# Performance work log

Hardware: AMD Instinct MI355X
Metric: run time of the kernel (lower is better)

The kernel has to match this reference:

```python
import jax, jax.numpy as jnp
import numpy as np

N_NODES = 50000
N_EDGES = 800000
NODE_DIM = 10
EDGE_DIM = 5
HID = 64


def _tconv(x, src, dst, e_attr, wq, bq, wk, bk, wv, bv, we, ws, bs):
    # PyG TransformerConv, heads=1, concat=True, root_weight=True, beta=False
    n = x.shape[0]
    q = x @ wq + bq                      # [N, HID]
    k = x @ wk + bk                      # [N, HID]
    v = x @ wv + bv                      # [N, HID]
    ee = e_attr @ we                     # [E, HID] (lin_edge, no bias)
    ke = k[src] + ee                     # key per edge
    ve = v[src] + ee                     # value per edge
    logits = jnp.sum(q[dst] * ke, axis=-1) / 8.0  # sqrt(64) = 8
    m = jax.ops.segment_max(logits, dst, num_segments=n)
    p = jnp.exp(logits - m[dst])
    s = jax.ops.segment_sum(p, dst, num_segments=n)
    alpha = p / s[dst]                   # segment softmax over in-neighbors
    agg = jax.ops.segment_sum(alpha[:, None] * ve, dst, num_segments=n)
    return agg + x @ ws + bs             # + lin_skip(x_i)


def setup_inputs() -> dict:
    key = jax.random.key(0)
    ks = jax.random.split(key, 32)
    x = jax.random.uniform(ks[0], (N_NODES, NODE_DIM), dtype=jnp.float32)
    edge_index = jax.random.randint(ks[1], (2, N_EDGES), 0, N_NODES, dtype=jnp.int64)
    edge_attr = jax.random.uniform(ks[2], (N_EDGES, EDGE_DIM), dtype=jnp.float32)

    def lin(k, fan_in, fan_out):
        b = 1.0 / np.sqrt(fan_in)
        return jax.random.uniform(k, (fan_in, fan_out), jnp.float32, -b, b)

    def bias(k, fan_in, fan_out):
        b = 1.0 / np.sqrt(fan_in)
        return jax.random.uniform(k, (fan_out,), jnp.float32, -b, b)

    inp = dict(x=x, edge_index=edge_index, edge_attr=edge_attr)
    # conv1: NODE_DIM -> HID
    inp['w1q'] = lin(ks[3], NODE_DIM, HID); inp['b1q'] = bias(ks[4], NODE_DIM, HID)
    inp['w1k'] = lin(ks[5], NODE_DIM, HID); inp['b1k'] = bias(ks[6], NODE_DIM, HID)
    inp['w1v'] = lin(ks[7], NODE_DIM, HID); inp['b1v'] = bias(ks[8], NODE_DIM, HID)
    inp['w1e'] = lin(ks[9], EDGE_DIM, HID)
    inp['w1s'] = lin(ks[10], NODE_DIM, HID); inp['b1s'] = bias(ks[11], NODE_DIM, HID)
    # 5 stacked HID -> HID layers
    inp['wq'] = jnp.stack([lin(jax.random.fold_in(ks[12], i), HID, HID) for i in range(5)])
    inp['bq'] = jnp.stack([bias(jax.random.fold_in(ks[13], i), HID, HID) for i in range(5)])
    inp['wk'] = jnp.stack([lin(jax.random.fold_in(ks[14], i), HID, HID) for i in range(5)])
    inp['bk'] = jnp.stack([bias(jax.random.fold_in(ks[15], i), HID, HID) for i in range(5)])
    inp['wv'] = jnp.stack([lin(jax.random.fold_in(ks[16], i), HID, HID) for i in range(5)])
    inp['bv'] = jnp.stack([bias(jax.random.fold_in(ks[17], i), HID, HID) for i in range(5)])
    inp['we'] = jnp.stack([lin(jax.random.fold_in(ks[18], i), EDGE_DIM, HID) for i in range(5)])
    inp['ws'] = jnp.stack([lin(jax.random.fold_in(ks[19], i), HID, HID) for i in range(5)])
    inp['bs'] = jnp.stack([bias(jax.random.fold_in(ks[20], i), HID, HID) for i in range(5)])
    # final linear HID -> 1
    inp['lin_w'] = lin(ks[21], HID, 1); inp['lin_b'] = bias(ks[22], HID, 1)
    return inp


def reference(x, edge_index, edge_attr, w1q, b1q, w1k, b1k, w1v, b1v, w1e, w1s, b1s,
              wq, bq, wk, bk, wv, bv, we, ws, bs, lin_w, lin_b):
    src, dst = edge_index[0], edge_index[1]  # x_j = x[src], aggregated into dst
    h = jnp.log(x + 1.0)
    e = jnp.log(edge_attr + 1.0)
    h = _tconv(h, src, dst, e, w1q, b1q, w1k, b1k, w1v, b1v, w1e, w1s, b1s)
    for i in range(5):
        h = _tconv(h, src, dst, e, wq[i], bq[i], wk[i], bk[i], wv[i], bv[i], we[i], ws[i], bs[i])
    return h @ lin_w + lin_b  # [N, 1]
```

## Files before the change

### kernel.cpp

```cpp
#include <hip/hip_runtime.h>
#include <hip/hip_fp16.h>
#include <cstdint>
#include <cstddef>

#define NN 50000
#define NE 800000
#define HD 64
#define SB 49

__global__ void k_hist(const int* __restrict__ ei, int* __restrict__ cnt) {
    int e = blockIdx.x * blockDim.x + threadIdx.x;
    if (e < NE) atomicAdd(&cnt[ei[NE + e]], 1);
}

__global__ __launch_bounds__(256) void k_scan1(const int* __restrict__ cnt,
                                               int* __restrict__ row_start,
                                               int* __restrict__ bsum) {
    __shared__ int ssum[256];
    const int tid = threadIdx.x, b = blockIdx.x;
    const int i0 = b * 1024 + tid * 4;
    int c0 = 0, c1 = 0, c2 = 0, c3 = 0;
    if (i0 + 3 < NN) {
        const int4 c = *(const int4*)(cnt + i0);
        c0 = c.x; c1 = c.y; c2 = c.z; c3 = c.w;
    } else {
        if (i0 + 0 < NN) c0 = cnt[i0 + 0];
        if (i0 + 1 < NN) c1 = cnt[i0 + 1];
        if (i0 + 2 < NN) c2 = cnt[i0 + 2];
        if (i0 + 3 < NN) c3 = cnt[i0 + 3];
    }
    ssum[tid] = c0 + c1 + c2 + c3;
    __syncthreads();
    for (int off = 1; off < 256; off <<= 1) {
        int v = (tid >= off) ? ssum[tid - off] : 0;
        __syncthreads();
        ssum[tid] += v;
        __syncthreads();
    }
    int ex = (tid == 0) ? 0 : ssum[tid - 1];
    if (i0 + 0 < NN) row_start[i0 + 0] = ex;
    ex += c0;
    if (i0 + 1 < NN) row_start[i0 + 1] = ex;
    ex += c1;
    if (i0 + 2 < NN) row_start[i0 + 2] = ex;
    ex += c2;
    if (i0 + 3 < NN) row_start[i0 + 3] = ex;
    if (tid == 255) bsum[b] = ssum[255];
}

__global__ __launch_bounds__(64) void k_scan2(const int* __restrict__ bsum,
                                              int* __restrict__ boff,
                                              int* __restrict__ row_start) {
    __shared__ int s[64];
    const int t = threadIdx.x;
    s[t] = (t < SB) ? bsum[t] : 0;
    __syncthreads();
    for (int off = 1; off < 64; off <<= 1) {
        int v = (t >= off) ? s[t - off] : 0;
        __syncthreads();
        s[t] += v;
        __syncthreads();
    }
    if (t < SB) boff[t] = (t == 0) ? 0 : s[t - 1];
    if (t == 0) row_start[NN] = s[SB - 1];
}

__global__ __launch_bounds__(256) void k_scan3(int* __restrict__ row_start,
                                               const int* __restrict__ boff,
                                               int* __restrict__ cur) {
    const int b = blockIdx.x;
    const int i0 = b * 1024 + threadIdx.x * 4;
    const int o = boff[b];
#pragma unroll
    for (int k = 0; k < 4; ++k) {
        int i = i0 + k;
        if (i < NN) {
            int v = row_start[i] + o;
            row_start[i] = v;
            cur[i] = v;
        }
    }
}

__global__ void k_scatter(const int* __restrict__ ei, const float* __restrict__ ea,
                          int* __restrict__ cur, uint4* __restrict__ e5p) {
    int e = blockIdx.x * blockDim.x + threadIdx.x;
    if (e < NE) {
        int d = ei[NE + e];
        int pos = atomicAdd(&cur[d], 1);
        const float e0 = __logf(ea[(size_t)e * 5 + 0] + 1.f);
        const float e1 = __logf(ea[(size_t)e * 5 + 1] + 1.f);
        const float e2 = __logf(ea[(size_t)e * 5 + 2] + 1.f);
        const float e3 = __logf(ea[(size_t)e * 5 + 3] + 1.f);
        const float e4 = __logf(ea[(size_t)e * 5 + 4] + 1.f);
        union { __half2 h; unsigned u; } c01, c23;
        c01.h = __floats2half2_rn(e0, e1);
        c23.h = __floats2half2_rn(e2, e3);
        uint4 rec;
        rec.x = c01.u;
        rec.y = c23.u;
        rec.z = ((unsigned)ei[e] << 16) |
                (unsigned)__half_as_ushort(__float2half_rn(e4));
        rec.w = 0u;
        e5p[pos] = rec;
    }
}

__device__ __forceinline__ void cvt_kv(const uint4 u, float4& k4, float4& v4) {
    const float2 p0 = __half22float2(*(const __half2*)&u.x);
    const float2 p1 = __half22float2(*(const __half2*)&u.y);
    const float2 p2 = __half22float2(*(const __half2*)&u.z);
    const float2 p3 = __half22float2(*(const __half2*)&u.w);
    k4 = make_float4(p0.x, p1.x, p2.x, p3.x);
    v4 = make_float4(p0.y, p1.y, p2.y, p3.y);
}

__global__ __launch_bounds__(256, 4) void k_qkvs10(
    const float* __restrict__ x,
    const float* __restrict__ Wq, const float* __restrict__ Bq,
    const float* __restrict__ Wk, const float* __restrict__ Bk,
    const float* __restrict__ Wv, const float* __restrict__ Bv,
    const float* __restrict__ Ws, const float* __restrict__ Bs,
    float* __restrict__ qb, __half* __restrict__ kvh, float* __restrict__ sb) {
    __shared__ float xs[640];
    const int lane = threadIdx.x & 63;
    const int w = threadIdx.x >> 6;
    const bool iskv = (w == 1 || w == 3);
    const float* WA = (w == 0) ? Wq : iskv ? Wk : Ws;
    const float* BA = (w == 0) ? Bq : iskv ? Bk : Bs;
    const float scl = (w == 0) ? 0.125f : 1.f;
    float wrA[10], wrB[10];
#pragma unroll
    for (int j = 0; j < 10; ++j) {
        wrA[j] = WA[j * 64 + lane] * scl;
        wrB[j] = iskv ? Wv[j * 64 + lane] : 0.f;
    }
    const float bA = BA[lane] * scl;
    const float bB = iskv ? Bv[lane] : 0.f;
    const int tile = blockIdx.x;
    const int fbase = tile * 640;
    const int fcnt = min(640, NN * 10 - fbase);
    if (threadIdx.x * 4 < fcnt) {
        float4 v = *(const float4*)(x + (size_t)fbase + threadIdx.x * 4);
        v.x = __logf(v.x + 1.f);
        v.y = __logf(v.y + 1.f);
        v.z = __logf(v.z + 1.f);
        v.w = __logf(v.w + 1.f);
        *(float4*)&xs[threadIdx.x * 4] = v;
    }
    __syncthreads();
    const int nbase = tile * 64;
    const int nodes = min(64, NN - nbase);
    const int n0 = (w == 3) ? 32 : 0;
    const int n1 = iskv ? ((w == 1) ? min(nodes, 32) : nodes) : nodes;
    for (int n = n0; n < n1; ++n) {
        float accA = bA, accB = bB;
#pragma unroll
        for (int j = 0; j < 10; ++j) {
            const float xv = xs[n * 10 + j];
            accA = fmaf(xv, wrA[j], accA);
            accB = fmaf(xv, wrB[j], accB);
        }
        const size_t node = (size_t)(nbase + n);
        if (iskv) {
            const __half2 hv = __floats2half2_rn(accA, accB);
            *(__half2*)(kvh + node * 128 + lane * 2) = hv;
        } else if (w == 0) {
            qb[node * 64 + lane] = accA;
        } else {
            sb[node * 64 + lane] = accA;
        }
    }
}

template <bool FINAL>
__global__ __launch_bounds__(256) void k_agg(
    const float* __restrict__ q, const __half* __restrict__ kv,
    const float* __restrict__ sk, const uint4* __restrict__ e5p,
    const float* __restrict__ wE, const int* __restrict__ row_start,
    float* __restrict__ hout, const float* __restrict__ lw, const float* lb,
    const float* __restrict__ Wq, const float* __restrict__ Bq,
    const float* __restrict__ Wk, const float* __restrict__ Bk,
    const float* __restrict__ Wv, const float* __restrict__ Bv,
    const float* __restrict__ Ws, const float* __restrict__ Bs,
    float* __restrict__ qout, __half* __restrict__ kvout,
    float* __restrict__ sout) {
    __shared__ float ols[256];
    __shared__ float kls[256];
    const int lane = threadIdx.x & 63;
    const int wave = threadIdx.x >> 6;
    const int g = lane >> 4, t = lane & 15;
    const int node = __builtin_amdgcn_readfirstlane(blockIdx.x * 4 + wave);
    const int beg = row_start[node], end = row_start[node + 1];
    const float4 s4 = *(const float4*)(sk + (size_t)node * 64 + t * 4);
    float4 o4;
    if (beg == end) {
        o4 = s4;
    } else {
        const float4 q4 = *(const float4*)(q + (size_t)node * 64 + t * 4);
        float g5[5];
        {
            const float4 wg = *(const float4*)(wE + g * 64 + t * 4);
            float dc = q4.x * wg.x;
            dc = fmaf(q4.y, wg.y, dc);
            dc = fmaf(q4.z, wg.z, dc);
            dc = fmaf(q4.w, wg.w, dc);
            dc += __shfl_xor(dc, 1);
            dc += __shfl_xor(dc, 2);
            dc += __shfl_xor(dc, 4);
            dc += __shfl_xor(dc, 8);
            const float4 w4 = *(const float4*)(wE + 4 * 64 + t * 4);
            float d4 = q4.x * w4.x;
            d4 = fmaf(q4.y, w4.y, d4);
            d4 = fmaf(q4.z, w4.z, d4);
            d4 = fmaf(q4.w, w4.w, d4);
            d4 += __shfl_xor(d4, 1);
            d4 += __shfl_xor(d4, 2);
            d4 += __shfl_xor(d4, 4);
            d4 += __shfl_xor(d4, 8);
            g5[0] = __shfl(dc, 0);
            g5[1] = __shfl(dc, 16);
            g5[2] = __shfl(dc, 32);
            g5[3] = __shfl(dc, 48);
            g5[4] = __shfl(d4, 0);
        }
        float m = -1e30f, l = 0.f;
        float4 accv = {0.f, 0.f, 0.f, 0.f};
        float a50 = 0.f, a51 = 0.f, a52 = 0.f, a53 = 0.f, a54 = 0.f;
        const char* kvc = (const char*)kv;
        const int i0x = beg + g;
        const int i0 = (i0x < end) ? i0x : beg;
        uint4 r0 = e5p[i0];
        const int i1x = beg + 4 + g;
        const int i1 = (i1x < end) ? i1x : beg;
        uint4 r1 = e5p[i1];
        uint4 kv8 =
            *(const uint4*)(kvc + (size_t)((r0.z & 0xffff0000u) >> 8) + t * 16);
#pragma unroll 2
        for (int p = beg; p < end; p += 4) {
            const int nx = p + 8 + g;
            const int npp = (nx < end) ? nx : beg;
            const uint4 rn = e5p[npp];
            const uint4 nkv =
                *(const uint4*)(kvc + (size_t)((r1.z & 0xffff0000u) >> 8) + t * 16);
            const bool act = (p + g) < end;
            float4 k4, v4;
            cvt_kv(kv8, k4, v4);
            const float2 e01 = __half22float2(*(const __half2*)&r0.x);
            const float2 e23 = __half22float2(*(const __half2*)&r0.y);
            const float e4v =
                __half2float(__ushort_as_half((unsigned short)(r0.z & 0xffffu)));
            float d = q4.x * k4.x;
            d = fmaf(q4.y, k4.y, d);
            d = fmaf(q4.z, k4.z, d);
            d = fmaf(q4.w, k4.w, d);
            d += __shfl_xor(d, 1);
            d += __shfl_xor(d, 2);
            d += __shfl_xor(d, 4);
            d += __shfl_xor(d, 8);
            float d5 = g5[0] * e01.x;
            d5 = fmaf(g5[1], e01.y, d5);
            d5 = fmaf(g5[2], e23.x, d5);
            d5 = fmaf(g5[3], e23.y, d5);
            d5 = fmaf(g5[4], e4v, d5);
            const float la = act ? (d + d5) : -__builtin_inff();
            float pa = __expf(la - m);
            if (la > m + 8.f) {
                const float rs = __expf(m - la);
                l *= rs;
                accv.x *= rs;
                accv.y *= rs;
                accv.z *= rs;
                accv.w *= rs;
                a50 *= rs;
                a51 *= rs;
                a52 *= rs;
                a53 *= rs;
                a54 *= rs;
                m = la;
                pa = 1.f;
            }
            l += pa;
            accv.x = fmaf(pa, v4.x, accv.x);
            accv.y = fmaf(pa, v4.y, accv.y);
            accv.z = fmaf(pa, v4.z, accv.z);
            accv.w = fmaf(pa, v4.w, accv.w);
            a50 = fmaf(pa, e01.x, a50);
            a51 = fmaf(pa, e01.y, a51);
            a52 = fmaf(pa, e23.x, a52);
            a53 = fmaf(pa, e23.y, a53);
            a54 = fmaf(pa, e4v, a54);
            r0 = r1;
            r1 = rn;
            kv8 = nkv;
        }
        float M = fmaxf(m, __shfl_xor(m, 16));
        M = fmaxf(M, __shfl_xor(M, 32));
        const float f = __expf(m - M);
        float lz = l * f;
        lz += __shfl_xor(lz, 16);
        lz += __shfl_xor(lz, 32);
        accv.x *= f;
        accv.y *= f;
        accv.z *= f;
        accv.w *= f;
        a50 *= f;
        a51 *= f;
        a52 *= f;
        a53 *= f;
        a54 *= f;
#pragma unroll
        for (int s = 16; s <= 32; s <<= 1) {
            accv.x += __shfl_xor(accv.x, s);
            accv.y += __shfl_xor(accv.y, s);
            accv.z += __shfl_xor(accv.z, s);
            accv.w += __shfl_xor(accv.w, s);
            a50 += __shfl_xor(a50, s);
            a51 += __shfl_xor(a51, s);
            a52 += __shfl_xor(a52, s);
            a53 += __shfl_xor(a53, s);
            a54 += __shfl_xor(a54, s);
        }
        float4 t4 = accv;
        {
            const float4 w0 = *(const float4*)(wE + 0 * 64 + t * 4);
            const float4 w1 = *(const float4*)(wE + 1 * 64 + t * 4);
            const float4 w2 = *(const float4*)(wE + 2 * 64 + t * 4);
            const float4 w3 = *(const float4*)(wE + 3 * 64 + t * 4);
            const float4 w4r = *(const float4*)(wE + 4 * 64 + t * 4);
            t4.x = fmaf(a50, w0.x, t4.x);
            t4.y = fmaf(a50, w0.y, t4.y);
            t4.z = fmaf(a50, w0.z, t4.z);
            t4.w = fmaf(a50, w0.w, t4.w);
            t4.x = fmaf(a51, w1.x, t4.x);
            t4.y = fmaf(a51, w1.y, t4.y);
            t4.z = fmaf(a51, w1.z, t4.z);
            t4.w = fmaf(a51, w1.w, t4.w);
            t4.x = fmaf(a52, w2.x, t4.x);
            t4.y = fmaf(a52, w2.y, t4.y);
            t4.z = fmaf(a52, w2.z, t4.z);
            t4.w = fmaf(a52, w2.w, t4.w);
            t4.x = fmaf(a53, w3.x, t4.x);
            t4.y = fmaf(a53, w3.y, t4.y);
            t4.z = fmaf(a53, w3.z, t4.z);
            t4.w = fmaf(a53, w3.w, t4.w);
            t4.x = fmaf(a54, w4r.x, t4.x);
            t4.y = fmaf(a54, w4r.y, t4.y);
            t4.z = fmaf(a54, w4r.z, t4.z);
            t4.w = fmaf(a54, w4r.w, t4.w);
        }
        const float rl = 1.f / lz;
        o4.x = fmaf(t4.x, rl, s4.x);
        o4.y = fmaf(t4.y, rl, s4.y);
        o4.z = fmaf(t4.z, rl, s4.z);
        o4.w = fmaf(t4.w, rl, s4.w);
    }
    if (FINAL) {
        const float4 lw4 = *(const float4*)(lw + t * 4);
        float r = o4.x * lw4.x;
        r = fmaf(o4.y, lw4.y, r);
        r = fmaf(o4.z, lw4.z, r);
        r = fmaf(o4.w, lw4.w, r);
        r += __shfl_xor(r, 1);
        r += __shfl_xor(r, 2);
        r += __shfl_xor(r, 4);
        r += __shfl_xor(r, 8);
        if (lane == 0) hout[node] = r + lb[0];
        return;
    }
    if (g == 0) *(float4*)&ols[wave * 64 + t * 4] = o4;
    __syncthreads();
    const float* W = (wave == 0) ? Wq : (wave == 1) ? Ws : (wave == 2) ? Wk : Wv;
    const float* B = (wave == 0) ? Bq : (wave == 1) ? Bs : (wave == 2) ? Bk : Bv;
    const float scl = (wave == 0) ? 0.125f : 1.f;
    float wr[64];
#pragma unroll
    for (int j = 0; j < 64; ++j) wr[j] = W[j * 64 + lane] * scl;
    const float bias = B[lane] * scl;
    float acc[4] = {bias, bias, bias, bias};
#pragma unroll
    for (int jq = 0; jq < 16; ++jq) {
#pragma unroll
        for (int n = 0; n < 4; ++n) {
            const float4 xv = *(const float4*)&ols[n * 64 + jq * 4];
            acc[n] = fmaf(xv.x, wr[jq * 4 + 0], acc[n]);
            acc[n] = fmaf(xv.y, wr[jq * 4 + 1], acc[n]);
            acc[n] = fmaf(xv.z, wr[jq * 4 + 2], acc[n]);
            acc[n] = fmaf(xv.w, wr[jq * 4 + 3], acc[n]);
        }
    }
    if (wave == 2) {
#pragma unroll
        for (int n = 0; n < 4; ++n) kls[n * 64 + lane] = acc[n];
    }
    __syncthreads();
    const int nb = blockIdx.x * 4;
    if (wave == 0) {
#pragma unroll
        for (int n = 0; n < 4; ++n) qout[(size_t)(nb + n) * 64 + lane] = acc[n];
    } else if (wave == 1) {
#pragma unroll
        for (int n = 0; n < 4; ++n) sout[(size_t)(nb + n) * 64 + lane] = acc[n];
    } else if (wave == 3) {
#pragma unroll
        for (int n = 0; n < 4; ++n) {
            const float kk = kls[n * 64 + lane];
            *(__half2*)(kvout + (size_t)(nb + n) * 128 + lane * 2) =
                __floats2half2_rn(kk, acc[n]);
        }
    }
}

extern "C" void kernel_launch(void* const* d_in, const int* in_sizes, int n_in,
                              void* d_out, int out_size, void* d_ws, size_t ws_size,
                              hipStream_t stream) {
    const float* x = (const float*)d_in[0];
    const int* ei = (const int*)d_in[1];
    const float* ea = (const float*)d_in[2];
    const float* w1q = (const float*)d_in[3];
    const float* b1q = (const float*)d_in[4];
    const float* w1k = (const float*)d_in[5];
    const float* b1k = (const float*)d_in[6];
    const float* w1v = (const float*)d_in[7];
    const float* b1v = (const float*)d_in[8];
    const float* w1e = (const float*)d_in[9];
    const float* w1s = (const float*)d_in[10];
    const float* b1s = (const float*)d_in[11];
    const float* wq = (const float*)d_in[12];
    const float* bq = (const float*)d_in[13];
    const float* wk = (const float*)d_in[14];
    const float* bk = (const float*)d_in[15];
    const float* wv = (const float*)d_in[16];
    const float* bv = (const float*)d_in[17];
    const float* we = (const float*)d_in[18];
    const float* ws = (const float*)d_in[19];
    const float* bs = (const float*)d_in[20];
    const float* lw = (const float*)d_in[21];
    const float* lb = (const float*)d_in[22];

    uintptr_t p = (uintptr_t)d_ws;
    auto alloc = [&](size_t bytes) -> void* {
        void* r = (void*)p;
        p += (bytes + 255) & ~(size_t)255;
        return r;
    };
    uint4* e5p = (uint4*)alloc((size_t)NE * 16);
    float* qA = (float*)alloc((size_t)NN * HD * 4);
    float* qB = (float*)alloc((size_t)NN * HD * 4);
    float* sA = (float*)alloc((size_t)NN * HD * 4);
    float* sB = (float*)alloc((size_t)NN * HD * 4);
    __half* kvA = (__half*)alloc((size_t)NN * 128 * 2);
    __half* kvB = (__half*)alloc((size_t)NN * 128 * 2);
    int* row_start = (int*)alloc((size_t)(NN + 1) * 4);
    int* cnt = (int*)alloc((size_t)NN * 4);
    int* cur = (int*)alloc((size_t)NN * 4);
    int* bsum = (int*)alloc((size_t)SB * 4);
    int* boff = (int*)alloc((size_t)SB * 4);

    hipMemsetAsync(cnt, 0, (size_t)NN * 4, stream);
    k_hist<<<(NE + 255) / 256, 256, 0, stream>>>(ei, cnt);
    k_scan1<<<SB, 256, 0, stream>>>(cnt, row_start, bsum);
    k_scan2<<<1, 64, 0, stream>>>(bsum, boff, row_start);
    k_scan3<<<SB, 256, 0, stream>>>(row_start, boff, cur);
    k_scatter<<<(NE + 255) / 256, 256, 0, stream>>>(ei, ea, cur, e5p);

    const int gg10 = (NN + 63) / 64;
    const int agg_grid = NN / 4;

    k_qkvs10<<<gg10, 256, 0, stream>>>(x, w1q, b1q, w1k, b1k, w1v, b1v, w1s, b1s,
                                       qA, kvA, sA);

    const float* wEs[6] = {w1e, we, we + 320, we + 640, we + 960, we + 1280};
    float* qin = qA;  float* qo = qB;
    float* sin_ = sA; float* so = sB;
    __half* kvin = kvA; __half* kvo = kvB;
    for (int k = 0; k < 5; ++k) {
        k_agg<false><<<agg_grid, 256, 0, stream>>>(
            qin, kvin, sin_, e5p, wEs[k], row_start, nullptr, lw, lb,
            wq + k * 4096, bq + k * 64, wk + k * 4096, bk + k * 64,
            wv + k * 4096, bv + k * 64, ws + k * 4096, bs + k * 64,
            qo, kvo, so);
        float* tf;  __half* th;
        tf = qin; qin = qo; qo = tf;
        tf = sin_; sin_ = so; so = tf;
        th = kvin; kvin = kvo; kvo = th;
    }
    k_agg<true><<<agg_grid, 256, 0, stream>>>(
        qin, kvin, sin_, e5p, wEs[5], row_start, (float*)d_out, lw, lb,
        wq, bq, wk, bk, wv, bv, ws, bs, qo, kvo, so);
}
```

Measured before the change: 620.9 us.

## Make aggregation kernel persistent and hoist per-wave weight loads out of node loop

The per-layer aggregation kernel becomes a grid-stride persistent kernel with 1024 blocks, each looping over groups of four nodes. The 64 per-lane weight registers for the fused next-layer projection are loaded once per block instead of once per four nodes, which cuts repeated weight traffic. Launch bounds now ask for 4 blocks per CU, which can constrain registers and cause spills given the 64-float weight array kept live across the loop. A fixed grid may also balance uneven node degrees worse than a large one-shot grid.

```diff
diff --git a/kernel.cpp b/kernel.cpp
--- a/kernel.cpp
+++ b/kernel.cpp
@@ -7,6 +7,7 @@
 #define NE 800000
 #define HD 64
 #define SB 49
+#define NQUAD 12500
 
 __global__ void k_hist(const int* __restrict__ ei, int* __restrict__ cnt) {
     int e = blockIdx.x * blockDim.x + threadIdx.x;
@@ -174,7 +175,7 @@
 }
 
 template <bool FINAL>
-__global__ __launch_bounds__(256) void k_agg(
+__global__ __launch_bounds__(256, 4) void k_agg(
     const float* __restrict__ q, const __half* __restrict__ kv,
     const float* __restrict__ sk, const uint4* __restrict__ e5p,
     const float* __restrict__ wE, const int* __restrict__ row_start,
@@ -190,223 +191,228 @@
     const int lane = threadIdx.x & 63;
     const int wave = threadIdx.x >> 6;
     const int g = lane >> 4, t = lane & 15;
-    const int node = __builtin_amdgcn_readfirstlane(blockIdx.x * 4 + wave);
-    const int beg = row_start[node], end = row_start[node + 1];
-    const float4 s4 = *(const float4*)(sk + (size_t)node * 64 + t * 4);
-    float4 o4;
-    if (beg == end) {
-        o4 = s4;
-    } else {
-        const float4 q4 = *(const float4*)(q + (size_t)node * 64 + t * 4);
-        float g5[5];
-        {
-            const float4 wg = *(const float4*)(wE + g * 64 + t * 4);
-            float dc = q4.x * wg.x;
-            dc = fmaf(q4.y, wg.y, dc);
-            dc = fmaf(q4.z, wg.z, dc);
-            dc = fmaf(q4.w, wg.w, dc);
-            dc += __shfl_xor(dc, 1);
-            dc += __shfl_xor(dc, 2);
-            dc += __shfl_xor(dc, 4);
-            dc += __shfl_xor(dc, 8);
-            const float4 w4 = *(const float4*)(wE + 4 * 64 + t * 4);
-            float d4 = q4.x * w4.x;
-            d4 = fmaf(q4.y, w4.y, d4);
-            d4 = fmaf(q4.z, w4.z, d4);
-            d4 = fmaf(q4.w, w4.w, d4);
-            d4 += __shfl_xor(d4, 1);
-            d4 += __shfl_xor(d4, 2);
-            d4 += __shfl_xor(d4, 4);
-            d4 += __shfl_xor(d4, 8);
-            g5[0] = __shfl(dc, 0);
-            g5[1] = __shfl(dc, 16);
-            g5[2] = __shfl(dc, 32);
-            g5[3] = __shfl(dc, 48);
-            g5[4] = __shfl(d4, 0);
-        }
-        float m = -1e30f, l = 0.f;
-        float4 accv = {0.f, 0.f, 0.f, 0.f};
-        float a50 = 0.f, a51 = 0.f, a52 = 0.f, a53 = 0.f, a54 = 0.f;
-        const char* kvc = (const char*)kv;
-        const int i0x = beg + g;
-        const int i0 = (i0x < end) ? i0x : beg;
-        uint4 r0 = e5p[i0];
-        const int i1x = beg + 4 + g;
-        const int i1 = (i1x < end) ? i1x : beg;
-        uint4 r1 = e5p[i1];
-        uint4 kv8 =
-            *(const uint4*)(kvc + (size_t)((r0.z & 0xffff0000u) >> 8) + t * 16);
+    float wr[64];
+    float bias = 0.f;
+    if (!FINAL) {
+        const float* W = (wave == 0) ? Wq : (wave == 1) ? Ws : (wave == 2) ? Wk : Wv;
+        const float* B = (wave == 0) ? Bq : (wave == 1) ? Bs : (wave == 2) ? Bk : Bv;
+        const float wscl = (wave == 0) ? 0.125f : 1.f;
+#pragma unroll
+        for (int j = 0; j < 64; ++j) wr[j] = W[j * 64 + lane] * wscl;
+        bias = B[lane] * wscl;
+    }
+    for (int quad = blockIdx.x; quad < NQUAD; quad += gridDim.x) {
+        const int node = __builtin_amdgcn_readfirstlane(quad * 4 + wave);
+        const int beg = row_start[node], end = row_start[node + 1];
+        const float4 s4 = *(const float4*)(sk + (size_t)node * 64 + t * 4);
+        float4 o4;
+        if (beg == end) {
+            o4 = s4;
+        } else {
+            const float4 q4 = *(const float4*)(q + (size_t)node * 64 + t * 4);
+            float g5[5];
+            {
+                const float4 wg = *(const float4*)(wE + g * 64 + t * 4);
+                float dc = q4.x * wg.x;
+                dc = fmaf(q4.y, wg.y, dc);
+                dc = fmaf(q4.z, wg.z, dc);
+                dc = fmaf(q4.w, wg.w, dc);
+                dc += __shfl_xor(dc, 1);
+                dc += __shfl_xor(dc, 2);
+                dc += __shfl_xor(dc, 4);
+                dc += __shfl_xor(dc, 8);
+                const float4 w4 = *(const float4*)(wE + 4 * 64 + t * 4);
+                float d4 = q4.x * w4.x;
+                d4 = fmaf(q4.y, w4.y, d4);
+                d4 = fmaf(q4.z, w4.z, d4);
+                d4 = fmaf(q4.w, w4.w, d4);
+                d4 += __shfl_xor(d4, 1);
+                d4 += __shfl_xor(d4, 2);
+                d4 += __shfl_xor(d4, 4);
+                d4 += __shfl_xor(d4, 8);
+                g5[0] = __shfl(dc, 0);
+                g5[1] = __shfl(dc, 16);
+                g5[2] = __shfl(dc, 32);
+                g5[3] = __shfl(dc, 48);
+                g5[4] = __shfl(d4, 0);
+            }
+            float m = -1e30f, l = 0.f;
+            float4 accv = {0.f, 0.f, 0.f, 0.f};
+            float a50 = 0.f, a51 = 0.f, a52 = 0.f, a53 = 0.f, a54 = 0.f;
+            const char* kvc = (const char*)kv;
+            const int i0x = beg + g;
+            const int i0 = (i0x < end) ? i0x : beg;
+            uint4 r0 = e5p[i0];
+            const int i1x = beg + 4 + g;
+            const int i1 = (i1x < end) ? i1x : beg;
+            uint4 r1 = e5p[i1];
+            uint4 kv8 =
+                *(const uint4*)(kvc + (size_t)((r0.z & 0xffff0000u) >> 8) + t * 16);
 #pragma unroll 2
-        for (int p = beg; p < end; p += 4) {
-            const int nx = p + 8 + g;
-            const int npp = (nx < end) ? nx : beg;
-            const uint4 rn = e5p[npp];
-            const uint4 nkv =
-                *(const uint4*)(kvc + (size_t)((r1.z & 0xffff0000u) >> 8) + t * 16);
-            const bool act = (p + g) < end;
-            float4 k4, v4;
-            cvt_kv(kv8, k4, v4);
-            const float2 e01 = __half22float2(*(const __half2*)&r0.x);
-            const float2 e23 = __half22float2(*(const __half2*)&r0.y);
-            const float e4v =
-                __half2float(__ushort_as_half((unsigned short)(r0.z & 0xffffu)));
-            float d = q4.x * k4.x;
-            d = fmaf(q4.y, k4.y, d);
-            d = fmaf(q4.z, k4.z, d);
-            d = fmaf(q4.w, k4.w, d);
-            d += __shfl_xor(d, 1);
-            d += __shfl_xor(d, 2);
-            d += __shfl_xor(d, 4);
-            d += __shfl_xor(d, 8);
-            float d5 = g5[0] * e01.x;
-            d5 = fmaf(g5[1], e01.y, d5);
-            d5 = fmaf(g5[2], e23.x, d5);
-            d5 = fmaf(g5[3], e23.y, d5);
-            d5 = fmaf(g5[4], e4v, d5);
-            const float la = act ? (d + d5) : -__builtin_inff();
-            float pa = __expf(la - m);
-            if (la > m + 8.f) {
-                const float rs = __expf(m - la);
-                l *= rs;
-                accv.x *= rs;
-                accv.y *= rs;
-                accv.z *= rs;
-                accv.w *= rs;
-                a50 *= rs;
-                a51 *= rs;
-                a52 *= rs;
-                a53 *= rs;
-                a54 *= rs;
-                m = la;
-                pa = 1.f;
-            }
-            l += pa;
-            accv.x = fmaf(pa, v4.x, accv.x);
-            accv.y = fmaf(pa, v4.y, accv.y);
-            accv.z = fmaf(pa, v4.z, accv.z);
-            accv.w = fmaf(pa, v4.w, accv.w);
-            a50 = fmaf(pa, e01.x, a50);
-            a51 = fmaf(pa, e01.y, a51);
-            a52 = fmaf(pa, e23.x, a52);
-            a53 = fmaf(pa, e23.y, a53);
-            a54 = fmaf(pa, e4v, a54);
-            r0 = r1;
-            r1 = rn;
-            kv8 = nkv;
-        }
-        float M = fmaxf(m, __shfl_xor(m, 16));
-        M = fmaxf(M, __shfl_xor(M, 32));
-        const float f = __expf(m - M);
-        float lz = l * f;
-        lz += __shfl_xor(lz, 16);
-        lz += __shfl_xor(lz, 32);
-        accv.x *= f;
-        accv.y *= f;
-        accv.z *= f;
-        accv.w *= f;
-        a50 *= f;
-        a51 *= f;
-        a52 *= f;
-        a53 *= f;
-        a54 *= f;
-#pragma unroll
-        for (int s = 16; s <= 32; s <<= 1) {
-            accv.x += __shfl_xor(accv.x, s);
-            accv.y += __shfl_xor(accv.y, s);
-            accv.z += __shfl_xor(accv.z, s);
-            accv.w += __shfl_xor(accv.w, s);
-            a50 += __shfl_xor(a50, s);
-            a51 += __shfl_xor(a51, s);
-            a52 += __shfl_xor(a52, s);
-            a53 += __shfl_xor(a53, s);
-            a54 += __shfl_xor(a54, s);
-        }
-        float4 t4 = accv;
-        {
-            const float4 w0 = *(const float4*)(wE + 0 * 64 + t * 4);
-            const float4 w1 = *(const float4*)(wE + 1 * 64 + t * 4);
-            const float4 w2 = *(const float4*)(wE + 2 * 64 + t * 4);
-            const float4 w3 = *(const float4*)(wE + 3 * 64 + t * 4);
-            const float4 w4r = *(const float4*)(wE + 4 * 64 + t * 4);
-            t4.x = fmaf(a50, w0.x, t4.x);
-            t4.y = fmaf(a50, w0.y, t4.y);
-            t4.z = fmaf(a50, w0.z, t4.z);
-            t4.w = fmaf(a50, w0.w, t4.w);
-            t4.x = fmaf(a51, w1.x, t4.x);
-            t4.y = fmaf(a51, w1.y, t4.y);
-            t4.z = fmaf(a51, w1.z, t4.z);
-            t4.w = fmaf(a51, w1.w, t4.w);
-            t4.x = fmaf(a52, w2.x, t4.x);
-            t4.y = fmaf(a52, w2.y, t4.y);
-            t4.z = fmaf(a52, w2.z, t4.z);
-            t4.w = fmaf(a52, w2.w, t4.w);
-            t4.x = fmaf(a53, w3.x, t4.x);
-            t4.y = fmaf(a53, w3.y, t4.y);
-            t4.z = fmaf(a53, w3.z, t4.z);
-            t4.w = fmaf(a53, w3.w, t4.w);
-            t4.x = fmaf(a54, w4r.x, t4.x);
-            t4.y = fmaf(a54, w4r.y, t4.y);
-            t4.z = fmaf(a54, w4r.z, t4.z);
-            t4.w = fmaf(a54, w4r.w, t4.w);
-        }
-        const float rl = 1.f / lz;
-        o4.x = fmaf(t4.x, rl, s4.x);
-        o4.y = fmaf(t4.y, rl, s4.y);
-        o4.z = fmaf(t4.z, rl, s4.z);
-        o4.w = fmaf(t4.w, rl, s4.w);
-    }
-    if (FINAL) {
-        const float4 lw4 = *(const float4*)(lw + t * 4);
-        float r = o4.x * lw4.x;
-        r = fmaf(o4.y, lw4.y, r);
-        r = fmaf(o4.z, lw4.z, r);
-        r = fmaf(o4.w, lw4.w, r);
-        r += __shfl_xor(r, 1);
-        r += __shfl_xor(r, 2);
-        r += __shfl_xor(r, 4);
-        r += __shfl_xor(r, 8);
-        if (lane == 0) hout[node] = r + lb[0];
-        return;
-    }
-    if (g == 0) *(float4*)&ols[wave * 64 + t * 4] = o4;
-    __syncthreads();
-    const float* W = (wave == 0) ? Wq : (wave == 1) ? Ws : (wave == 2) ? Wk : Wv;
-    const float* B = (wave == 0) ? Bq : (wave == 1) ? Bs : (wave == 2) ? Bk : Bv;
-    const float scl = (wave == 0) ? 0.125f : 1.f;
-    float wr[64];
-#pragma unroll
-    for (int j = 0; j < 64; ++j) wr[j] = W[j * 64 + lane] * scl;
-    const float bias = B[lane] * scl;
-    float acc[4] = {bias, bias, bias, bias};
-#pragma unroll
-    for (int jq = 0; jq < 16; ++jq) {
-#pragma unroll
-        for (int n = 0; n < 4; ++n) {
-            const float4 xv = *(const float4*)&ols[n * 64 + jq * 4];
-            acc[n] = fmaf(xv.x, wr[jq * 4 + 0], acc[n]);
-            acc[n] = fmaf(xv.y, wr[jq * 4 + 1], acc[n]);
-            acc[n] = fmaf(xv.z, wr[jq * 4 + 2], acc[n]);
-            acc[n] = fmaf(xv.w, wr[jq * 4 + 3], acc[n]);
-        }
-    }
-    if (wave == 2) {
-#pragma unroll
-        for (int n = 0; n < 4; ++n) kls[n * 64 + lane] = acc[n];
-    }
-    __syncthreads();
-    const int nb = blockIdx.x * 4;
-    if (wave == 0) {
-#pragma unroll
-        for (int n = 0; n < 4; ++n) qout[(size_t)(nb + n) * 64 + lane] = acc[n];
-    } else if (wave == 1) {
-#pragma unroll
-        for (int n = 0; n < 4; ++n) sout[(size_t)(nb + n) * 64 + lane] = acc[n];
-    } else if (wave == 3) {
-#pragma unroll
-        for (int n = 0; n < 4; ++n) {
-            const float kk = kls[n * 64 + lane];
-            *(__half2*)(kvout + (size_t)(nb + n) * 128 + lane * 2) =
-                __floats2half2_rn(kk, acc[n]);
+            for (int p = beg; p < end; p += 4) {
+                const int nx = p + 8 + g;
+                const int npp = (nx < end) ? nx : beg;
+                const uint4 rn = e5p[npp];
+                const uint4 nkv = *(const uint4*)(
+                    kvc + (size_t)((r1.z & 0xffff0000u) >> 8) + t * 16);
+                const bool act = (p + g) < end;
+                float4 k4, v4;
+                cvt_kv(kv8, k4, v4);
+                const float2 e01 = __half22float2(*(const __half2*)&r0.x);
+                const float2 e23 = __half22float2(*(const __half2*)&r0.y);
+                const float e4v =
+                    __half2float(__ushort_as_half((unsigned short)(r0.z & 0xffffu)));
+                float d = q4.x * k4.x;
+                d = fmaf(q4.y, k4.y, d);
+                d = fmaf(q4.z, k4.z, d);
+                d = fmaf(q4.w, k4.w, d);
+                d += __shfl_xor(d, 1);
+                d += __shfl_xor(d, 2);
+                d += __shfl_xor(d, 4);
+                d += __shfl_xor(d, 8);
+                float d5 = g5[0] * e01.x;
+                d5 = fmaf(g5[1], e01.y, d5);
+                d5 = fmaf(g5[2], e23.x, d5);
+                d5 = fmaf(g5[3], e23.y, d5);
+                d5 = fmaf(g5[4], e4v, d5);
+                const float la = act ? (d + d5) : -__builtin_inff();
+                float pa = __expf(la - m);
+                if (la > m + 8.f) {
+                    const float rs = __expf(m - la);
+                    l *= rs;
+                    accv.x *= rs;
+                    accv.y *= rs;
+                    accv.z *= rs;
+                    accv.w *= rs;
+                    a50 *= rs;
+                    a51 *= rs;
+                    a52 *= rs;
+                    a53 *= rs;
+                    a54 *= rs;
+                    m = la;
+                    pa = 1.f;
+                }
+                l += pa;
+                accv.x = fmaf(pa, v4.x, accv.x);
+                accv.y = fmaf(pa, v4.y, accv.y);
+                accv.z = fmaf(pa, v4.z, accv.z);
+                accv.w = fmaf(pa, v4.w, accv.w);
+                a50 = fmaf(pa, e01.x, a50);
+                a51 = fmaf(pa, e01.y, a51);
+                a52 = fmaf(pa, e23.x, a52);
+                a53 = fmaf(pa, e23.y, a53);
+                a54 = fmaf(pa, e4v, a54);
+                r0 = r1;
+                r1 = rn;
+                kv8 = nkv;
+            }
+            float M = fmaxf(m, __shfl_xor(m, 16));
+            M = fmaxf(M, __shfl_xor(M, 32));
+            const float f = __expf(m - M);
+            float lz = l * f;
+            lz += __shfl_xor(lz, 16);
+            lz += __shfl_xor(lz, 32);
+            accv.x *= f;
+            accv.y *= f;
+            accv.z *= f;
+            accv.w *= f;
+            a50 *= f;
+            a51 *= f;
+            a52 *= f;
+            a53 *= f;
+            a54 *= f;
+#pragma unroll
+            for (int s = 16; s <= 32; s <<= 1) {
+                accv.x += __shfl_xor(accv.x, s);
+                accv.y += __shfl_xor(accv.y, s);
+                accv.z += __shfl_xor(accv.z, s);
+                accv.w += __shfl_xor(accv.w, s);
+                a50 += __shfl_xor(a50, s);
+                a51 += __shfl_xor(a51, s);
+                a52 += __shfl_xor(a52, s);
+                a53 += __shfl_xor(a53, s);
+                a54 += __shfl_xor(a54, s);
+            }
+            float4 t4 = accv;
+            {
+                const float4 w0 = *(const float4*)(wE + 0 * 64 + t * 4);
+                const float4 w1 = *(const float4*)(wE + 1 * 64 + t * 4);
+                const float4 w2 = *(const float4*)(wE + 2 * 64 + t * 4);
+                const float4 w3 = *(const float4*)(wE + 3 * 64 + t * 4);
+                const float4 w4r = *(const float4*)(wE + 4 * 64 + t * 4);
+                t4.x = fmaf(a50, w0.x, t4.x);
+                t4.y = fmaf(a50, w0.y, t4.y);
+                t4.z = fmaf(a50, w0.z, t4.z);
+                t4.w = fmaf(a50, w0.w, t4.w);
+                t4.x = fmaf(a51, w1.x, t4.x);
+                t4.y = fmaf(a51, w1.y, t4.y);
+                t4.z = fmaf(a51, w1.z, t4.z);
+                t4.w = fmaf(a51, w1.w, t4.w);
+                t4.x = fmaf(a52, w2.x, t4.x);
+                t4.y = fmaf(a52, w2.y, t4.y);
+                t4.z = fmaf(a52, w2.z, t4.z);
+                t4.w = fmaf(a52, w2.w, t4.w);
+                t4.x = fmaf(a53, w3.x, t4.x);
+                t4.y = fmaf(a53, w3.y, t4.y);
+                t4.z = fmaf(a53, w3.z, t4.z);
+                t4.w = fmaf(a53, w3.w, t4.w);
+                t4.x = fmaf(a54, w4r.x, t4.x);
+                t4.y = fmaf(a54, w4r.y, t4.y);
+                t4.z = fmaf(a54, w4r.z, t4.z);
+                t4.w = fmaf(a54, w4r.w, t4.w);
+            }
+            const float rl = 1.f / lz;
+            o4.x = fmaf(t4.x, rl, s4.x);
+            o4.y = fmaf(t4.y, rl, s4.y);
+            o4.z = fmaf(t4.z, rl, s4.z);
+            o4.w = fmaf(t4.w, rl, s4.w);
+        }
+        if (FINAL) {
+            const float4 lw4 = *(const float4*)(lw + t * 4);
+            float r = o4.x * lw4.x;
+            r = fmaf(o4.y, lw4.y, r);
+            r = fmaf(o4.z, lw4.z, r);
+            r = fmaf(o4.w, lw4.w, r);
+            r += __shfl_xor(r, 1);
+            r += __shfl_xor(r, 2);
+            r += __shfl_xor(r, 4);
+            r += __shfl_xor(r, 8);
+            if (lane == 0) hout[node] = r + lb[0];
+            continue;
+        }
+        if (g == 0) *(float4*)&ols[wave * 64 + t * 4] = o4;
+        __syncthreads();
+        float acc[4] = {bias, bias, bias, bias};
+#pragma unroll
+        for (int jq = 0; jq < 16; ++jq) {
+#pragma unroll
+            for (int n = 0; n < 4; ++n) {
+                const float4 xv = *(const float4*)&ols[n * 64 + jq * 4];
+                acc[n] = fmaf(xv.x, wr[jq * 4 + 0], acc[n]);
+                acc[n] = fmaf(xv.y, wr[jq * 4 + 1], acc[n]);
+                acc[n] = fmaf(xv.z, wr[jq * 4 + 2], acc[n]);
+                acc[n] = fmaf(xv.w, wr[jq * 4 + 3], acc[n]);
+            }
+        }
+        if (wave == 2) {
+#pragma unroll
+            for (int n = 0; n < 4; ++n) kls[n * 64 + lane] = acc[n];
+        }
+        __syncthreads();
+        const int nb = quad * 4;
+        if (wave == 0) {
+#pragma unroll
+            for (int n = 0; n < 4; ++n) qout[(size_t)(nb + n) * 64 + lane] = acc[n];
+        } else if (wave == 1) {
+#pragma unroll
+            for (int n = 0; n < 4; ++n) sout[(size_t)(nb + n) * 64 + lane] = acc[n];
+        } else if (wave == 3) {
+#pragma unroll
+            for (int n = 0; n < 4; ++n) {
+                const float kk = kls[n * 64 + lane];
+                *(__half2*)(kvout + (size_t)(nb + n) * 128 + lane * 2) =
+                    __floats2half2_rn(kk, acc[n]);
+            }
         }
     }
 }
@@ -465,7 +471,7 @@
     k_scatter<<<(NE + 255) / 256, 256, 0, stream>>>(ei, ea, cur, e5p);
 
     const int gg10 = (NN + 63) / 64;
-    const int agg_grid = NN / 4;
+    const int persist_grid = 1024;
 
     k_qkvs10<<<gg10, 256, 0, stream>>>(x, w1q, b1q, w1k, b1k, w1v, b1v, w1s, b1s,
                                        qA, kvA, sA);
@@ -475,7 +481,7 @@
     float* sin_ = sA; float* so = sB;
     __half* kvin = kvA; __half* kvo = kvB;
     for (int k = 0; k < 5; ++k) {
-        k_agg<false><<<agg_grid, 256, 0, stream>>>(
+        k_agg<false><<<persist_grid, 256, 0, stream>>>(
             qin, kvin, sin_, e5p, wEs[k], row_start, nullptr, lw, lb,
             wq + k * 4096, bq + k * 64, wk + k * 4096, bk + k * 64,
             wv + k * 4096, bv + k * 64, ws + k * 4096, bs + k * 64,
@@ -485,7 +491,7 @@
         tf = sin_; sin_ = so; so = tf;
         th = kvin; kvin = kvo; kvo = th;
     }
-    k_agg<true><<<agg_grid, 256, 0, stream>>>(
+    k_agg<true><<<NQUAD, 256, 0, stream>>>(
         qin, kvin, sin_, e5p, wEs[5], row_start, (float*)d_out, lw, lb,
         wq, bq, wk, bk, wv, bv, ws, bs, qo, kvo, so);
 }
```

Result: slower. 746.7 us (+20.3%).
